# Performance work log

Measured on AMD Instinct MI355X. Metric: run time of the kernel, lower is better.

## Reference

```python
import jax, jax.numpy as jnp
import numpy as np

N = 50000
E = 800000
NODE_IN = 16
EDGE_IN = 8
HID = 128
OUT = 128
HEADS = 4
HC = HID // HEADS          # per-head channels = 32
EH = HID // 2              # edge hidden = 64
EPS = 1e-5
NEG_SLOPE = 0.2            # PyG GATConv leaky_relu slope


def setup_inputs() -> dict:
    key = jax.random.key(0)
    ks = list(jax.random.split(key, 16))
    it = iter(ks)
    nx = lambda: next(it)
    s = 0.05
    p = {}
    p["x"] = jax.random.normal(nx(), (N, NODE_IN), jnp.float32)
    p["edge_index"] = jax.random.randint(nx(), (2, E), 0, N)
    p["edge_attr"] = jax.random.normal(nx(), (E, EDGE_IN), jnp.float32)
    # node_preprocess: Linear + LayerNorm
    p["np_w"] = jax.random.normal(nx(), (NODE_IN, HID), jnp.float32) * s
    p["np_b"] = jnp.zeros((HID,), jnp.float32)
    p["np_g"] = jnp.ones((HID,), jnp.float32)
    p["np_be"] = jnp.zeros((HID,), jnp.float32)
    # edge_preprocess: Linear + LayerNorm
    p["ep_w"] = jax.random.normal(nx(), (EDGE_IN, EH), jnp.float32) * s
    p["ep_b"] = jnp.zeros((EH,), jnp.float32)
    p["ep_g"] = jnp.ones((EH,), jnp.float32)
    p["ep_be"] = jnp.zeros((EH,), jnp.float32)
    # 3 stacked GATConv layers (params stacked on leading dim)
    p["gat_w"] = jax.random.normal(nx(), (3, HID, HID), jnp.float32) * s
    p["gat_as"] = jax.random.normal(nx(), (3, HEADS, HC), jnp.float32) * s
    p["gat_ad"] = jax.random.normal(nx(), (3, HEADS, HC), jnp.float32) * s
    p["gat_ew"] = jax.random.normal(nx(), (3, EH, HID), jnp.float32) * s
    p["gat_ae"] = jax.random.normal(nx(), (3, HEADS, HC), jnp.float32) * s
    p["gat_b"] = jnp.zeros((3, HID), jnp.float32)
    # BatchNorm affine params
    p["bn_g"] = jnp.ones((3, HID), jnp.float32)
    p["bn_b"] = jnp.zeros((3, HID), jnp.float32)
    # final_proj: Linear + LayerNorm
    p["fp_w"] = jax.random.normal(nx(), (HID, OUT), jnp.float32) * s
    p["fp_b"] = jnp.zeros((OUT,), jnp.float32)
    p["fp_g"] = jnp.ones((OUT,), jnp.float32)
    p["fp_be"] = jnp.zeros((OUT,), jnp.float32)
    return p


def _ln(x, g, b):
    m = x.mean(-1, keepdims=True)
    v = ((x - m) ** 2).mean(-1, keepdims=True)
    return (x - m) * jax.lax.rsqrt(v + EPS) * g + b


def _bn(x, g, b):  # training-mode batch statistics over node dim
    m = x.mean(0)
    v = ((x - m) ** 2).mean(0)
    return (x - m) * jax.lax.rsqrt(v + EPS) * g + b


def _gat(h, e, src, dst, W, a_s, a_d, We, a_e, bias):
    # h: [N, HID], e: [E2, EH], src/dst: [E2]
    xs = (h @ W).reshape(N, HEADS, HC)                       # [N,H,C]
    al_s = (xs * a_s).sum(-1)                                # [N,H]
    al_d = (xs * a_d).sum(-1)                                # [N,H]
    eh = (e @ We).reshape(-1, HEADS, HC)                     # [E2,H,C]
    alpha = al_s[src] + al_d[dst] + (eh * a_e).sum(-1)       # [E2,H]
    alpha = jnp.where(alpha >= 0, alpha, NEG_SLOPE * alpha)  # leaky relu
    # segment softmax over incoming edges of each dst node
    amax = jax.ops.segment_max(alpha, dst, num_segments=N)
    ex = jnp.exp(alpha - amax[dst])
    w = ex / jax.ops.segment_sum(ex, dst, num_segments=N)[dst]
    msg = xs[src] * w[:, :, None]                            # [E2,H,C]
    out = jax.ops.segment_sum(msg, dst, num_segments=N)      # [N,H,C]
    return out.reshape(N, HID) + bias


def reference(x, edge_index, edge_attr, np_w, np_b, np_g, np_be,
              ep_w, ep_b, ep_g, ep_be,
              gat_w, gat_as, gat_ad, gat_ew, gat_ae, gat_b,
              bn_g, bn_b, fp_w, fp_b, fp_g, fp_be):
    src, dst = edge_index[0], edge_index[1]
    h = jax.nn.relu(_ln(x @ np_w + np_b, np_g, np_be))
    e = jax.nn.relu(_ln(edge_attr @ ep_w + ep_b, ep_g, ep_be))
    # PyG GATConv default add_self_loops=True, fill_value='mean':
    # self-loop edge_attr = mean of incoming edge_attr per dst node (0 if none)
    deg = jax.ops.segment_sum(jnp.ones((E,), e.dtype), dst, num_segments=N)
    loop_e = jax.ops.segment_sum(e, dst, num_segments=N) / jnp.maximum(deg, 1.0)[:, None]
    ar = jnp.arange(N)
    src2 = jnp.concatenate([src, ar])
    dst2 = jnp.concatenate([dst, ar])
    e2 = jnp.concatenate([e, loop_e], axis=0)
    for i in range(3):
        res = h
        h = _gat(h, e2, src2, dst2, gat_w[i], gat_as[i], gat_ad[i],
                 gat_ew[i], gat_ae[i], gat_b[i])
        h = jax.nn.relu(_bn(h, bn_g[i], bn_b[i]) + res)
    return _ln(h @ fp_w + fp_b, fp_g, fp_be)
```

## Files before the change

kernel.cpp:

```cpp
#include <hip/hip_runtime.h>
#include <hip/hip_bf16.h>
#include <math.h>

#define N_NODES 50000
#define N_EDGES 800000
#define EPS 1e-5f
#define SLOPE 0.2f

typedef unsigned int u32;
typedef unsigned short u16;
typedef float floatx4 __attribute__((ext_vector_type(4)));
typedef short short8_t __attribute__((ext_vector_type(8)));

__device__ __forceinline__ float bf2f(u16 v) {
    u32 u = ((u32)v) << 16;
    return __uint_as_float(u);
}
__device__ __forceinline__ u16 f2bf(float f) {
    u32 u = __float_as_uint(f);
    u32 r = (u + 0x7fffu + ((u >> 16) & 1u)) >> 16;
    return (u16)r;
}
__device__ __forceinline__ float lo_bf(u32 v) { return __uint_as_float(v << 16); }
__device__ __forceinline__ float hi_bf(u32 v) { return __uint_as_float(v & 0xffff0000u); }
__device__ __forceinline__ float wred(float v) {
    #pragma unroll
    for (int off = 32; off > 0; off >>= 1) v += __shfl_xor(v, off, 64);
    return v;
}

__global__ void k_prep(const float* __restrict__ w, u16* __restrict__ hi,
                       u16* __restrict__ lo, const float* __restrict__ ew,
                       const float* __restrict__ ae, float* __restrict__ M) {
    int b = blockIdx.x;
    if (b < 192) {
        int i = b * 256 + threadIdx.x;
        int l = i >> 14, r = i & 16383;
        int n = r >> 7, k = r & 127;
        float f = w[(size_t)l * 16384 + k * 128 + n];
        u16 hb = f2bf(f);
        hi[i] = hb;
        lo[i] = f2bf(f - bf2f(hb));
    } else {
        int t = (b - 192) * 256 + threadIdx.x;
        if (t >= 768) return;
        int k = t / 12, j = t % 12;
        int l = j >> 2, h = j & 3;
        const float* ewp = ew + l * 8192 + k * 128 + h * 32;
        const float* aep = ae + l * 128 + h * 32;
        float s = 0.f;
        #pragma unroll
        for (int c = 0; c < 32; c++) s += ewp[c] * aep[c];
        M[k * 12 + j] = s;
    }
}

__global__ __launch_bounds__(256) void k_node_pre(
        const float* __restrict__ x, const float* __restrict__ w,
        const float* __restrict__ b, const float* __restrict__ g,
        const float* __restrict__ be, float* __restrict__ h) {
    int wave = threadIdx.x >> 6, lane = threadIdx.x & 63;
    int n = blockIdx.x * 4 + wave;
    if (n >= N_NODES) return;
    const float* xr = x + (size_t)n * 16;
    float xv[16];
    #pragma unroll
    for (int k = 0; k < 16; k++) xv[k] = xr[k];
    int c0 = lane, c1 = lane + 64;
    float a0 = b[c0], a1 = b[c1];
    #pragma unroll
    for (int k = 0; k < 16; k++) {
        a0 = fmaf(xv[k], w[k * 128 + c0], a0);
        a1 = fmaf(xv[k], w[k * 128 + c1], a1);
    }
    float m = wred(a0 + a1) * (1.f / 128.f);
    float d0 = a0 - m, d1 = a1 - m;
    float v = wred(d0 * d0 + d1 * d1) * (1.f / 128.f);
    float rs = rsqrtf(v + EPS);
    float o0 = d0 * rs * g[c0] + be[c0];
    float o1 = d1 * rs * g[c1] + be[c1];
    h[(size_t)n * 128 + c0] = fmaxf(o0, 0.f);
    h[(size_t)n * 128 + c1] = fmaxf(o1, 0.f);
}

__global__ void k_deg(const int* __restrict__ dst, int* __restrict__ deg,
                      int* __restrict__ rank) {
    int e = blockIdx.x * 256 + threadIdx.x;
    if (e < N_EDGES) rank[e] = atomicAdd(&deg[dst[e]], 1);
}

__global__ void k_scan1(const int* __restrict__ deg, int* __restrict__ incl,
                        int* __restrict__ bsum) {
    __shared__ int lds[1024];
    int i = blockIdx.x * 1024 + threadIdx.x;
    int v = (i < N_NODES) ? deg[i] : 0;
    lds[threadIdx.x] = v;
    __syncthreads();
    for (int off = 1; off < 1024; off <<= 1) {
        int t = (threadIdx.x >= off) ? lds[threadIdx.x - off] : 0;
        __syncthreads();
        lds[threadIdx.x] += t;
        __syncthreads();
    }
    if (i < N_NODES) incl[i] = lds[threadIdx.x];
    if (threadIdx.x == 1023) bsum[blockIdx.x] = lds[1023];
}
__global__ void k_scan3(const int* __restrict__ incl, const int* __restrict__ bsum,
                        int* __restrict__ rowptr) {
    __shared__ int base_s;
    if (threadIdx.x == 0) {
        int acc = 0;
        for (int i = 0; i < (int)blockIdx.x; i++) acc += bsum[i];
        base_s = acc;
    }
    __syncthreads();
    int i = blockIdx.x * 1024 + threadIdx.x;
    if (i < N_NODES) rowptr[i + 1] = incl[i] + base_s;
    if (i == 0) rowptr[0] = 0;
}

__global__ void k_fill(const int* __restrict__ ei, const int* __restrict__ rowptr,
                       const int* __restrict__ rank, int2* __restrict__ csr_se,
                       const float* __restrict__ fw, u16* __restrict__ fhi,
                       u16* __restrict__ flo) {
    int b = blockIdx.x;
    if (b < 3125) {
        int e = b * 256 + threadIdx.x;
        if (e >= N_EDGES) return;
        int src = ei[e], dst = ei[N_EDGES + e];
        int slot = rowptr[dst] + rank[e];
        csr_se[slot] = make_int2(src, e);
    } else {
        int i = (b - 3125) * 256 + threadIdx.x;
        int n = i >> 7, k = i & 127;
        float f = fw[k * 128 + n];
        u16 hb = f2bf(f);
        fhi[i] = hb;
        flo[i] = f2bf(f - bf2f(hb));
    }
}

__global__ __launch_bounds__(256) void k_edge_c(
        const int2* __restrict__ csr_se, const float* __restrict__ ea,
        const float* __restrict__ epw, const float* __restrict__ epb,
        const float* __restrict__ epg, const float* __restrict__ epbe,
        const float* __restrict__ M, int* __restrict__ csr_src,
        float* __restrict__ csr_aE) {
    __shared__ floatx4 sW4[128], sM4[192], sB4[16], sG4[16], sBe4[16];
    int tid = threadIdx.x;
    if (tid < 128) sW4[tid] = ((const floatx4*)epw)[tid];
    if (tid < 192) sM4[tid] = ((const floatx4*)M)[tid];
    if (tid < 16) sB4[tid] = ((const floatx4*)epb)[tid];
    if (tid >= 32 && tid < 48) sG4[tid - 32] = ((const floatx4*)epg)[tid - 32];
    if (tid >= 64 && tid < 80) sBe4[tid - 64] = ((const floatx4*)epbe)[tid - 64];
    __syncthreads();
    int s = blockIdx.x * 256 + tid;
    if (s >= N_EDGES) return;
    int2 se = csr_se[s];
    int src = se.x, e = se.y;
    float4 x0 = *(const float4*)(ea + (size_t)e * 8);
    float4 x1 = *(const float4*)(ea + (size_t)e * 8 + 4);
    float xa[8] = {x0.x, x0.y, x0.z, x0.w, x1.x, x1.y, x1.z, x1.w};
    floatx4 v4[16];
    floatx4 sum4 = {0.f, 0.f, 0.f, 0.f};
    #pragma unroll
    for (int c4 = 0; c4 < 16; c4++) {
        floatx4 a = sB4[c4];
        #pragma unroll
        for (int k = 0; k < 8; k++) a += xa[k] * sW4[k * 16 + c4];
        v4[c4] = a;
        sum4 += a;
    }
    float m = (sum4[0] + sum4[1] + sum4[2] + sum4[3]) * (1.f / 64.f);
    floatx4 var4 = {0.f, 0.f, 0.f, 0.f};
    #pragma unroll
    for (int c4 = 0; c4 < 16; c4++) { floatx4 d = v4[c4] - m; var4 += d * d; }
    float rs = rsqrtf((var4[0] + var4[1] + var4[2] + var4[3]) * (1.f / 64.f) + EPS);
    #pragma unroll
    for (int c4 = 0; c4 < 16; c4++) {
        floatx4 o = (v4[c4] - m) * rs * sG4[c4] + sBe4[c4];
        #pragma unroll
        for (int p = 0; p < 4; p++) v4[c4][p] = fmaxf(o[p], 0.f);
    }
    floatx4 aE0 = {0.f, 0.f, 0.f, 0.f};
    floatx4 aE1 = {0.f, 0.f, 0.f, 0.f};
    floatx4 aE2 = {0.f, 0.f, 0.f, 0.f};
    #pragma unroll
    for (int c = 0; c < 64; c++) {
        float vc = v4[c >> 2][c & 3];
        aE0 += vc * sM4[c * 3 + 0];
        aE1 += vc * sM4[c * 3 + 1];
        aE2 += vc * sM4[c * 3 + 2];
    }
    csr_src[s] = src;
    *(floatx4*)(csr_aE + ((size_t)0 * N_EDGES + s) * 4) = aE0;
    *(floatx4*)(csr_aE + ((size_t)1 * N_EDGES + s) * 4) = aE1;
    *(floatx4*)(csr_aE + ((size_t)2 * N_EDGES + s) * 4) = aE2;
}

__global__ __launch_bounds__(256) void k_gemm_xs_mfma(
        float* __restrict__ h, const float* __restrict__ buf,
        const float* __restrict__ stats, const float* __restrict__ bng,
        const float* __restrict__ bnb, const u16* __restrict__ wt_hi,
        const u16* __restrict__ wt_lo, u16* __restrict__ xs, int fuse) {
    int wave = threadIdx.x >> 6, lane = threadIdx.x & 63;
    int r0 = (blockIdx.x * 4 + wave) * 16;
    if (r0 >= N_NODES) return;
    int lrow = lane & 15, lk = lane >> 4;
    size_t rowoff = (size_t)(r0 + lrow) * 128 + lk * 8;
    float* hp = h + rowoff;
    const float* bp = buf + rowoff;
    const u16* bph = wt_hi + lrow * 128 + lk * 8;
    const u16* bpl = wt_lo + lrow * 128 + lk * 8;
    floatx4 acc[8];
    #pragma unroll
    for (int j = 0; j < 8; j++) acc[j] = (floatx4){0.f, 0.f, 0.f, 0.f};
    #pragma unroll
    for (int s = 0; s < 4; s++) {
        float av[8];
        float4 h0 = *(const float4*)(hp + s * 32);
        float4 h1 = *(const float4*)(hp + s * 32 + 4);
        float hv[8] = {h0.x, h0.y, h0.z, h0.w, h1.x, h1.y, h1.z, h1.w};
        if (fuse) {
            float4 b0 = *(const float4*)(bp + s * 32);
            float4 b1 = *(const float4*)(bp + s * 32 + 4);
            float bv[8] = {b0.x, b0.y, b0.z, b0.w, b1.x, b1.y, b1.z, b1.w};
            #pragma unroll
            for (int i = 0; i < 8; i++) {
                int c = lk * 8 + s * 32 + i;
                float m = stats[c] * (1.f / N_NODES);
                float var = stats[128 + c] * (1.f / N_NODES) - m * m;
                float rsn = rsqrtf(var + EPS);
                float val = (bv[i] - m) * rsn * bng[c] + bnb[c] + hv[i];
                av[i] = fmaxf(val, 0.f);
            }
            float4 w0, w1;
            w0.x = av[0]; w0.y = av[1]; w0.z = av[2]; w0.w = av[3];
            w1.x = av[4]; w1.y = av[5]; w1.z = av[6]; w1.w = av[7];
            *(float4*)(hp + s * 32) = w0;
            *(float4*)(hp + s * 32 + 4) = w1;
        } else {
            #pragma unroll
            for (int i = 0; i < 8; i++) av[i] = hv[i];
        }
        short8_t ahi, alo;
        #pragma unroll
        for (int i = 0; i < 8; i++) {
            u16 hb = f2bf(av[i]);
            ahi[i] = (short)hb;
            alo[i] = (short)f2bf(av[i] - bf2f(hb));
        }
        short8_t bh[8], bl[8];
        #pragma unroll
        for (int j = 0; j < 8; j++) {
            bh[j] = *(const short8_t*)(bph + s * 32 + j * 2048);
            bl[j] = *(const short8_t*)(bpl + s * 32 + j * 2048);
        }
        #pragma unroll
        for (int j = 0; j < 8; j++)
            acc[j] = __builtin_amdgcn_mfma_f32_16x16x32_bf16(ahi, bh[j], acc[j], 0, 0, 0);
        #pragma unroll
        for (int j = 0; j < 8; j++)
            acc[j] = __builtin_amdgcn_mfma_f32_16x16x32_bf16(ahi, bl[j], acc[j], 0, 0, 0);
        #pragma unroll
        for (int j = 0; j < 8; j++)
            acc[j] = __builtin_amdgcn_mfma_f32_16x16x32_bf16(alo, bh[j], acc[j], 0, 0, 0);
    }
    u16* orow = xs + (size_t)(r0 + lk * 4) * 128 + lrow;
    #pragma unroll
    for (int j = 0; j < 8; j++) {
        #pragma unroll
        for (int reg = 0; reg < 4; reg++)
            orow[(size_t)reg * 128 + j * 16] = f2bf(acc[j][reg]);
    }
}

__global__ void k_al(const u16* __restrict__ xs, const float* __restrict__ as_,
                     const float* __restrict__ ad_, float* __restrict__ al_s,
                     float* __restrict__ al_d) {
    int t = blockIdx.x * 256 + threadIdx.x;
    if (t >= N_NODES * 4) return;
    int n = t >> 2, hh = t & 3;
    const uint4* xp = (const uint4*)(xs + (size_t)n * 128 + hh * 32);
    const float* app = as_ + hh * 32;
    const float* dpp = ad_ + hh * 32;
    float s = 0.f, d = 0.f;
    #pragma unroll
    for (int q = 0; q < 4; q++) {
        uint4 v = xp[q];
        u32 wv[4] = {v.x, v.y, v.z, v.w};
        #pragma unroll
        for (int p = 0; p < 4; p++) {
            int c = q * 8 + p * 2;
            float fl = lo_bf(wv[p]), fh = hi_bf(wv[p]);
            s = fmaf(fl, app[c], s); s = fmaf(fh, app[c + 1], s);
            d = fmaf(fl, dpp[c], d); d = fmaf(fh, dpp[c + 1], d);
        }
    }
    al_s[t] = s; al_d[t] = d;
}

__global__ __launch_bounds__(256) void k_agg(
        const int* __restrict__ rowptr, const int* __restrict__ csr_src,
        const float* __restrict__ aEl, const float* __restrict__ al_s,
        const float* __restrict__ al_d, const u16* __restrict__ xs,
        const float* __restrict__ bias, float* __restrict__ outp) {
    int lane = threadIdx.x & 63;
    int n = __builtin_amdgcn_readfirstlane(blockIdx.x * 4 + (threadIdx.x >> 6));
    if (n >= N_NODES) return;
    int row = rowptr[n], end = rowptr[n + 1];
    int hh = lane >> 4;
    const u32* xsw = (const u32*)xs;
    float ald = al_d[n * 4 + hh];
    float asn = al_s[n * 4 + hh];
    u32 xnp = xsw[(size_t)n * 64 + lane];
    float acc0 = 0.f, acc1 = 0.f, ssum = 0.f, aes = 0.f;
    int slot = row;
    for (; slot + 8 <= end; slot += 8) {
        int sv[8]; float ae[8], asv[8]; u32 xv[8];
        #pragma unroll
        for (int i = 0; i < 8; i++) sv[i] = csr_src[slot + i];
        #pragma unroll
        for (int i = 0; i < 8; i++) ae[i] = aEl[(size_t)(slot + i) * 4 + hh];
        #pragma unroll
        for (int i = 0; i < 8; i++) asv[i] = al_s[sv[i] * 4 + hh];
        #pragma unroll
        for (int i = 0; i < 8; i++) xv[i] = xsw[(size_t)sv[i] * 64 + lane];
        #pragma unroll
        for (int i = 0; i < 8; i++) {
            aes += ae[i];
            float a = asv[i] + ald + ae[i]; a = (a >= 0.f) ? a : SLOPE * a;
            float ev = __expf(a);
            ssum += ev;
            acc0 = fmaf(ev, lo_bf(xv[i]), acc0);
            acc1 = fmaf(ev, hi_bf(xv[i]), acc1);
        }
    }
    for (; slot + 4 <= end; slot += 4) {
        int sv[4]; float ae[4], asv[4]; u32 xv[4];
        #pragma unroll
        for (int i = 0; i < 4; i++) sv[i] = csr_src[slot + i];
        #pragma unroll
        for (int i = 0; i < 4; i++) ae[i] = aEl[(size_t)(slot + i) * 4 + hh];
        #pragma unroll
        for (int i = 0; i < 4; i++) asv[i] = al_s[sv[i] * 4 + hh];
        #pragma unroll
        for (int i = 0; i < 4; i++) xv[i] = xsw[(size_t)sv[i] * 64 + lane];
        #pragma unroll
        for (int i = 0; i < 4; i++) {
            aes += ae[i];
            float a = asv[i] + ald + ae[i]; a = (a >= 0.f) ? a : SLOPE * a;
            float ev = __expf(a);
            ssum += ev;
            acc0 = fmaf(ev, lo_bf(xv[i]), acc0);
            acc1 = fmaf(ev, hi_bf(xv[i]), acc1);
        }
    }
    for (; slot < end; slot++) {
        int sA = csr_src[slot];
        float aeA = aEl[(size_t)slot * 4 + hh];
        float asA = al_s[sA * 4 + hh];
        u32 xA = xsw[(size_t)sA * 64 + lane];
        aes += aeA;
        float aA = asA + ald + aeA; aA = (aA >= 0.f) ? aA : SLOPE * aA;
        float eA = __expf(aA);
        ssum += eA;
        acc0 = fmaf(eA, lo_bf(xA), acc0); acc1 = fmaf(eA, hi_bf(xA), acc1);
    }
    float dinv = 1.f / fmaxf((float)(end - row), 1.f);
    float sa = asn + ald + aes * dinv; sa = (sa >= 0.f) ? sa : SLOPE * sa;
    float e = __expf(sa);
    ssum += e;
    acc0 = fmaf(e, lo_bf(xnp), acc0); acc1 = fmaf(e, hi_bf(xnp), acc1);
    float2 bv = *(const float2*)(bias + lane * 2);
    float2 o;
    o.x = acc0 / ssum + bv.x;
    o.y = acc1 / ssum + bv.y;
    *(float2*)(outp + (size_t)n * 128 + lane * 2) = o;
}

__global__ void k_bn_stats(const float* __restrict__ x, float* __restrict__ stats) {
    __shared__ float lds[512];
    int t = threadIdx.x;
    int c = t & 127, half = t >> 7;
    float s = 0.f, q = 0.f;
    for (int n = blockIdx.x * 2 + half; n < N_NODES; n += gridDim.x * 2) {
        float v = x[(size_t)n * 128 + c];
        s += v; q = fmaf(v, v, q);
    }
    lds[t] = s; lds[256 + t] = q;
    __syncthreads();
    if (t < 128) {
        atomicAdd(&stats[c], lds[t] + lds[t + 128]);
        atomicAdd(&stats[128 + c], lds[256 + t] + lds[256 + t + 128]);
    }
}

__global__ __launch_bounds__(256) void k_gemm_fp_mfma(
        const float* __restrict__ h, const float* __restrict__ buf,
        const float* __restrict__ stats, const float* __restrict__ bng,
        const float* __restrict__ bnb, const u16* __restrict__ wt_hi,
        const u16* __restrict__ wt_lo, const float* __restrict__ fb,
        const float* __restrict__ g, const float* __restrict__ be,
        float* __restrict__ out) {
    int wave = threadIdx.x >> 6, lane = threadIdx.x & 63;
    int r0 = (blockIdx.x * 4 + wave) * 16;
    if (r0 >= N_NODES) return;
    int lrow = lane & 15, lk = lane >> 4;
    size_t rowoff = (size_t)(r0 + lrow) * 128 + lk * 8;
    const float* hp = h + rowoff;
    const float* bp = buf + rowoff;
    const u16* bph = wt_hi + lrow * 128 + lk * 8;
    const u16* bpl = wt_lo + lrow * 128 + lk * 8;
    floatx4 acc[8];
    #pragma unroll
    for (int j = 0; j < 8; j++) acc[j] = (floatx4){0.f, 0.f, 0.f, 0.f};
    #pragma unroll
    for (int s = 0; s < 4; s++) {
        float4 h0 = *(const float4*)(hp + s * 32);
        float4 h1 = *(const float4*)(hp + s * 32 + 4);
        float4 b0 = *(const float4*)(bp + s * 32);
        float4 b1 = *(const float4*)(bp + s * 32 + 4);
        float hv[8] = {h0.x, h0.y, h0.z, h0.w, h1.x, h1.y, h1.z, h1.w};
        float bvv[8] = {b0.x, b0.y, b0.z, b0.w, b1.x, b1.y, b1.z, b1.w};
        float av[8];
        #pragma unroll
        for (int i = 0; i < 8; i++) {
            int c = lk * 8 + s * 32 + i;
            float m = stats[c] * (1.f / N_NODES);
            float var = stats[128 + c] * (1.f / N_NODES) - m * m;
            float rsn = rsqrtf(var + EPS);
            float val = (bvv[i] - m) * rsn * bng[c] + bnb[c] + hv[i];
            av[i] = fmaxf(val, 0.f);
        }
        short8_t ahi, alo;
        #pragma unroll
        for (int i = 0; i < 8; i++) {
            u16 hb = f2bf(av[i]);
            ahi[i] = (short)hb;
            alo[i] = (short)f2bf(av[i] - bf2f(hb));
        }
        short8_t bh[8], bl[8];
        #pragma unroll
        for (int j = 0; j < 8; j++) {
            bh[j] = *(const short8_t*)(bph + s * 32 + j * 2048);
            bl[j] = *(const short8_t*)(bpl + s * 32 + j * 2048);
        }
        #pragma unroll
        for (int j = 0; j < 8; j++)
            acc[j] = __builtin_amdgcn_mfma_f32_16x16x32_bf16(ahi, bh[j], acc[j], 0, 0, 0);
        #pragma unroll
        for (int j = 0; j < 8; j++)
            acc[j] = __builtin_amdgcn_mfma_f32_16x16x32_bf16(ahi, bl[j], acc[j], 0, 0, 0);
        #pragma unroll
        for (int j = 0; j < 8; j++)
            acc[j] = __builtin_amdgcn_mfma_f32_16x16x32_bf16(alo, bh[j], acc[j], 0, 0, 0);
    }
    float gv[8], bev[8];
    #pragma unroll
    for (int j = 0; j < 8; j++) {
        float fbv = fb[j * 16 + lrow];
        gv[j] = g[j * 16 + lrow];
        bev[j] = be[j * 16 + lrow];
        #pragma unroll
        for (int reg = 0; reg < 4; reg++) acc[j][reg] += fbv;
    }
    float s1[4] = {0.f, 0.f, 0.f, 0.f}, s2[4] = {0.f, 0.f, 0.f, 0.f};
    #pragma unroll
    for (int j = 0; j < 8; j++) {
        #pragma unroll
        for (int reg = 0; reg < 4; reg++) {
            float y = acc[j][reg];
            s1[reg] += y;
            s2[reg] = fmaf(y, y, s2[reg]);
        }
    }
    #pragma unroll
    for (int off = 1; off <= 8; off <<= 1) {
        #pragma unroll
        for (int reg = 0; reg < 4; reg++) {
            s1[reg] += __shfl_xor(s1[reg], off, 64);
            s2[reg] += __shfl_xor(s2[reg], off, 64);
        }
    }
    #pragma unroll
    for (int reg = 0; reg < 4; reg++) {
        float m = s1[reg] * (1.f / 128.f);
        float var = s2[reg] * (1.f / 128.f) - m * m;
        float rs = rsqrtf(var + EPS);
        float* orow = out + (size_t)(r0 + lk * 4 + reg) * 128 + lrow;
        #pragma unroll
        for (int j = 0; j < 8; j++)
            orow[j * 16] = (acc[j][reg] - m) * rs * gv[j] + bev[j];
    }
}

extern "C" void kernel_launch(void* const* d_in, const int* in_sizes, int n_in,
                              void* d_out, int out_size, void* d_ws, size_t ws_size,
                              hipStream_t stream) {
    const float* x      = (const float*)d_in[0];
    const int*   ei     = (const int*)d_in[1];
    const float* ea     = (const float*)d_in[2];
    const float* np_w   = (const float*)d_in[3];
    const float* np_b   = (const float*)d_in[4];
    const float* np_g   = (const float*)d_in[5];
    const float* np_be  = (const float*)d_in[6];
    const float* ep_w   = (const float*)d_in[7];
    const float* ep_b   = (const float*)d_in[8];
    const float* ep_g   = (const float*)d_in[9];
    const float* ep_be  = (const float*)d_in[10];
    const float* gat_w  = (const float*)d_in[11];
    const float* gat_as = (const float*)d_in[12];
    const float* gat_ad = (const float*)d_in[13];
    const float* gat_ew = (const float*)d_in[14];
    const float* gat_ae = (const float*)d_in[15];
    const float* gat_b  = (const float*)d_in[16];
    const float* bn_g   = (const float*)d_in[17];
    const float* bn_b   = (const float*)d_in[18];
    const float* fp_w   = (const float*)d_in[19];
    const float* fp_b   = (const float*)d_in[20];
    const float* fp_g   = (const float*)d_in[21];
    const float* fp_be  = (const float*)d_in[22];
    float* out = (float*)d_out;

    char* ws = (char*)d_ws;
    size_t off = 0;
    auto alloc = [&](size_t bytes) -> void* {
        void* p = ws + off;
        off = (off + bytes + 255) & ~(size_t)255;
        return p;
    };
    float* h      = (float*)alloc((size_t)N_NODES * 128 * 4);
    float* buf    = (float*)alloc((size_t)N_NODES * 128 * 4);
    u16*   xs     = (u16*)alloc((size_t)N_NODES * 128 * 2);
    float* al_s   = (float*)alloc((size_t)N_NODES * 4 * 4);
    float* al_d   = (float*)alloc((size_t)N_NODES * 4 * 4);
    int*   deg    = (int*)alloc((size_t)N_NODES * 4);
    int*   rowptr = (int*)alloc((size_t)(N_NODES + 1) * 4);
    int*   cursor = (int*)alloc((size_t)N_NODES * 4);
    int*   incl   = (int*)alloc((size_t)N_NODES * 4);
    int*   bsum   = (int*)alloc(64 * 4);
    int*   csr_src= (int*)alloc((size_t)N_EDGES * 4);
    float* csr_aE = (float*)alloc((size_t)N_EDGES * 12 * 4);
    float* M      = (float*)alloc(64 * 12 * 4);
    float* stats  = (float*)alloc(256 * 4);
    u16*   wt_hi  = (u16*)alloc((size_t)3 * 16384 * 2);
    u16*   wt_lo  = (u16*)alloc((size_t)3 * 16384 * 2);
    (void)stats;
    int2*  csr_se = (int2*)buf;
    int*   rank   = (int*)xs;
    u16*   wtf_hi = (u16*)incl;
    u16*   wtf_lo = wtf_hi + 16384;
    float* stats3 = (float*)cursor;

    hipMemsetAsync(deg, 0, (size_t)N_NODES * 4, stream);
    hipMemsetAsync(stats3, 0, 3 * 256 * 4, stream);

    k_prep<<<195, 256, 0, stream>>>(gat_w, wt_hi, wt_lo, gat_ew, gat_ae, M);
    k_node_pre<<<(N_NODES + 3) / 4, 256, 0, stream>>>(x, np_w, np_b, np_g, np_be, h);
    k_deg<<<(N_EDGES + 255) / 256, 256, 0, stream>>>(ei + N_EDGES, deg, rank);
    int nblk = (N_NODES + 1023) / 1024;
    k_scan1<<<nblk, 1024, 0, stream>>>(deg, incl, bsum);
    k_scan3<<<nblk, 1024, 0, stream>>>(incl, bsum, rowptr);
    k_fill<<<3189, 256, 0, stream>>>(ei, rowptr, rank, csr_se, fp_w, wtf_hi, wtf_lo);
    k_edge_c<<<(N_EDGES + 255) / 256, 256, 0, stream>>>(csr_se, ea, ep_w, ep_b, ep_g,
                                                        ep_be, M, csr_src, csr_aE);

    for (int l = 0; l < 3; l++) {
        k_gemm_xs_mfma<<<(3125 + 3) / 4, 256, 0, stream>>>(
            h, buf, stats3 + (l > 0 ? (l - 1) * 256 : 0),
            bn_g + (l > 0 ? (l - 1) * 128 : 0),
            bn_b + (l > 0 ? (l - 1) * 128 : 0),
            wt_hi + (size_t)l * 16384, wt_lo + (size_t)l * 16384, xs, l > 0 ? 1 : 0);
        k_al<<<(N_NODES * 4 + 255) / 256, 256, 0, stream>>>(xs, gat_as + l * 128,
                                                            gat_ad + l * 128, al_s, al_d);
        k_agg<<<(N_NODES + 3) / 4, 256, 0, stream>>>(rowptr, csr_src,
                                                     csr_aE + (size_t)l * N_EDGES * 4,
                                                     al_s, al_d, xs, gat_b + l * 128, buf);
        k_bn_stats<<<256, 256, 0, stream>>>(buf, stats3 + l * 256);
    }
    k_gemm_fp_mfma<<<(3125 + 3) / 4, 256, 0, stream>>>(
        h, buf, stats3 + 2 * 256, bn_g + 2 * 128, bn_b + 2 * 128,
        wtf_hi, wtf_lo, fp_b, fp_g, fp_be, out);
}
```

Baseline: 661.6 us.

## Merge prep, node preprocess and degree kernels; add 16-edge unroll in aggregation

Three independent setup kernels (weight split, node preprocessing, degree counting) are folded into a single launch that dispatches on block index. This removes two kernel launches and the idle gaps between them. Separately, the aggregation loop gains a 16-edge unrolled stage ahead of the 8-edge one, so more gathers are in flight per wave. The wider unroll raises register pressure and may lower occupancy.

```diff
diff --git a/kernel.cpp b/kernel.cpp
--- a/kernel.cpp
+++ b/kernel.cpp
@@ -29,12 +29,45 @@
     return v;
 }
 
-__global__ void k_prep(const float* __restrict__ w, u16* __restrict__ hi,
-                       u16* __restrict__ lo, const float* __restrict__ ew,
-                       const float* __restrict__ ae, float* __restrict__ M) {
+#define NP_BLKS 12500
+#define DEG_BLKS 3125
+__global__ __launch_bounds__(256) void k_prep(
+        const float* __restrict__ x, const float* __restrict__ npw,
+        const float* __restrict__ npb, const float* __restrict__ npg,
+        const float* __restrict__ npbe, float* __restrict__ h,
+        const int* __restrict__ dst, int* __restrict__ deg, int* __restrict__ rank,
+        const float* __restrict__ w, u16* __restrict__ hi, u16* __restrict__ lo,
+        const float* __restrict__ ew, const float* __restrict__ ae,
+        float* __restrict__ M) {
     int b = blockIdx.x;
-    if (b < 192) {
-        int i = b * 256 + threadIdx.x;
+    if (b < NP_BLKS) {
+        int wave = threadIdx.x >> 6, lane = threadIdx.x & 63;
+        int n = b * 4 + wave;
+        if (n >= N_NODES) return;
+        const float* xr = x + (size_t)n * 16;
+        float xv[16];
+        #pragma unroll
+        for (int k = 0; k < 16; k++) xv[k] = xr[k];
+        int c0 = lane, c1 = lane + 64;
+        float a0 = npb[c0], a1 = npb[c1];
+        #pragma unroll
+        for (int k = 0; k < 16; k++) {
+            a0 = fmaf(xv[k], npw[k * 128 + c0], a0);
+            a1 = fmaf(xv[k], npw[k * 128 + c1], a1);
+        }
+        float m = wred(a0 + a1) * (1.f / 128.f);
+        float d0 = a0 - m, d1 = a1 - m;
+        float v = wred(d0 * d0 + d1 * d1) * (1.f / 128.f);
+        float rs = rsqrtf(v + EPS);
+        float o0 = d0 * rs * npg[c0] + npbe[c0];
+        float o1 = d1 * rs * npg[c1] + npbe[c1];
+        h[(size_t)n * 128 + c0] = fmaxf(o0, 0.f);
+        h[(size_t)n * 128 + c1] = fmaxf(o1, 0.f);
+    } else if (b < NP_BLKS + DEG_BLKS) {
+        int e = (b - NP_BLKS) * 256 + threadIdx.x;
+        if (e < N_EDGES) rank[e] = atomicAdd(&deg[dst[e]], 1);
+    } else if (b < NP_BLKS + DEG_BLKS + 192) {
+        int i = (b - NP_BLKS - DEG_BLKS) * 256 + threadIdx.x;
         int l = i >> 14, r = i & 16383;
         int n = r >> 7, k = r & 127;
         float f = w[(size_t)l * 16384 + k * 128 + n];
@@ -42,51 +75,17 @@
         hi[i] = hb;
         lo[i] = f2bf(f - bf2f(hb));
     } else {
-        int t = (b - 192) * 256 + threadIdx.x;
+        int t = (b - NP_BLKS - DEG_BLKS - 192) * 256 + threadIdx.x;
         if (t >= 768) return;
         int k = t / 12, j = t % 12;
-        int l = j >> 2, h = j & 3;
-        const float* ewp = ew + l * 8192 + k * 128 + h * 32;
-        const float* aep = ae + l * 128 + h * 32;
+        int l = j >> 2, hh = j & 3;
+        const float* ewp = ew + l * 8192 + k * 128 + hh * 32;
+        const float* aep = ae + l * 128 + hh * 32;
         float s = 0.f;
         #pragma unroll
         for (int c = 0; c < 32; c++) s += ewp[c] * aep[c];
         M[k * 12 + j] = s;
     }
-}
-
-__global__ __launch_bounds__(256) void k_node_pre(
-        const float* __restrict__ x, const float* __restrict__ w,
-        const float* __restrict__ b, const float* __restrict__ g,
-        const float* __restrict__ be, float* __restrict__ h) {
-    int wave = threadIdx.x >> 6, lane = threadIdx.x & 63;
-    int n = blockIdx.x * 4 + wave;
-    if (n >= N_NODES) return;
-    const float* xr = x + (size_t)n * 16;
-    float xv[16];
-    #pragma unroll
-    for (int k = 0; k < 16; k++) xv[k] = xr[k];
-    int c0 = lane, c1 = lane + 64;
-    float a0 = b[c0], a1 = b[c1];
-    #pragma unroll
-    for (int k = 0; k < 16; k++) {
-        a0 = fmaf(xv[k], w[k * 128 + c0], a0);
-        a1 = fmaf(xv[k], w[k * 128 + c1], a1);
-    }
-    float m = wred(a0 + a1) * (1.f / 128.f);
-    float d0 = a0 - m, d1 = a1 - m;
-    float v = wred(d0 * d0 + d1 * d1) * (1.f / 128.f);
-    float rs = rsqrtf(v + EPS);
-    float o0 = d0 * rs * g[c0] + be[c0];
-    float o1 = d1 * rs * g[c1] + be[c1];
-    h[(size_t)n * 128 + c0] = fmaxf(o0, 0.f);
-    h[(size_t)n * 128 + c1] = fmaxf(o1, 0.f);
-}
-
-__global__ void k_deg(const int* __restrict__ dst, int* __restrict__ deg,
-                      int* __restrict__ rank) {
-    int e = blockIdx.x * 256 + threadIdx.x;
-    if (e < N_EDGES) rank[e] = atomicAdd(&deg[dst[e]], 1);
 }
 
 __global__ void k_scan1(const int* __restrict__ deg, int* __restrict__ incl,
@@ -316,6 +315,26 @@
     u32 xnp = xsw[(size_t)n * 64 + lane];
     float acc0 = 0.f, acc1 = 0.f, ssum = 0.f, aes = 0.f;
     int slot = row;
+    for (; slot + 16 <= end; slot += 16) {
+        int sv[16]; float ae[16], asv[16]; u32 xv[16];
+        #pragma unroll
+        for (int i = 0; i < 16; i++) sv[i] = csr_src[slot + i];
+        #pragma unroll
+        for (int i = 0; i < 16; i++) ae[i] = aEl[(size_t)(slot + i) * 4 + hh];
+        #pragma unroll
+        for (int i = 0; i < 16; i++) asv[i] = al_s[sv[i] * 4 + hh];
+        #pragma unroll
+        for (int i = 0; i < 16; i++) xv[i] = xsw[(size_t)sv[i] * 64 + lane];
+        #pragma unroll
+        for (int i = 0; i < 16; i++) {
+            aes += ae[i];
+            float a = asv[i] + ald + ae[i]; a = (a >= 0.f) ? a : SLOPE * a;
+            float ev = __expf(a);
+            ssum += ev;
+            acc0 = fmaf(ev, lo_bf(xv[i]), acc0);
+            acc1 = fmaf(ev, hi_bf(xv[i]), acc1);
+        }
+    }
     for (; slot + 8 <= end; slot += 8) {
         int sv[8]; float ae[8], asv[8]; u32 xv[8];
         #pragma unroll
@@ -556,9 +575,10 @@
     hipMemsetAsync(deg, 0, (size_t)N_NODES * 4, stream);
     hipMemsetAsync(stats3, 0, 3 * 256 * 4, stream);
 
-    k_prep<<<195, 256, 0, stream>>>(gat_w, wt_hi, wt_lo, gat_ew, gat_ae, M);
-    k_node_pre<<<(N_NODES + 3) / 4, 256, 0, stream>>>(x, np_w, np_b, np_g, np_be, h);
-    k_deg<<<(N_EDGES + 255) / 256, 256, 0, stream>>>(ei + N_EDGES, deg, rank);
+    k_prep<<<NP_BLKS + DEG_BLKS + 195, 256, 0, stream>>>(
+        x, np_w, np_b, np_g, np_be, h,
+        ei + N_EDGES, deg, rank,
+        gat_w, wt_hi, wt_lo, gat_ew, gat_ae, M);
     int nblk = (N_NODES + 1023) / 1024;
     k_scan1<<<nblk, 1024, 0, stream>>>(deg, incl, bsum);
     k_scan3<<<nblk, 1024, 0, stream>>>(incl, bsum, rowptr);
```

New measurement: 684.6 us. 1.03x slower.
